# Optimization experiments

Measured on AMD Instinct MI355X. Metric: run time of the kernel, lower is better.

## Reference

```python
import math
import jax, jax.numpy as jnp
import numpy as np

B, S, D, H = 2, 4096, 512, 8
DH = D // H


def setup_inputs() -> dict:
    key = jax.random.key(0)
    ks = jax.random.split(key, 12)
    lim = 1.0 / math.sqrt(D)
    u = lambda k, shp: jax.random.uniform(k, shp, jnp.float32, -lim, lim)
    return {
        "x": jax.random.normal(ks[0], (B, S, D), jnp.float32),
        "gamma": jax.random.uniform(ks[1], (B, S, 1), jnp.float32),
        "Wq": u(ks[2], (D, D)), "bq": u(ks[3], (D,)),
        "Wk": u(ks[4], (D, D)), "bk": u(ks[5], (D,)),
        "Wv": u(ks[6], (D, D)), "bv": u(ks[7], (D,)),
        "Wo": u(ks[8], (D, D)), "bo": u(ks[9], (D,)),
    }


def reference(x, gamma, Wq, bq, Wk, bk, Wv, bv, Wo, bo):
    b, s, d = x.shape
    # projections (torch Linear: x @ W.T + b), split heads -> [B,H,S,DH]
    def proj(W, bias):
        return (x @ W.T + bias).reshape(b, s, H, DH).transpose(0, 2, 1, 3)
    q, k, v = proj(Wq, bq), proj(Wk, bk), proj(Wv, bv)

    scores = jnp.einsum("bhsd,bhtd->bhst", q, k) / math.sqrt(DH)  # [B,H,S,S]
    causal = jnp.triu(jnp.ones((s, s), bool), k=1)  # True above diagonal
    neg_inf = jnp.float32(-jnp.inf)
    scores = jnp.where(causal[None, None], neg_inf, scores)

    # hyperbolic positional bias: -log1p(gamma_i * max(i-j, 0) + 1e-8)
    pos = jnp.arange(s)
    delta = jnp.clip(pos[:, None] - pos[None, :], 0).astype(jnp.float32)  # [S,S]
    gamma_q = gamma[:, :, 0][:, :, None]  # [B,S,1]
    hyper = -jnp.log1p(gamma_q * delta + 1e-8)  # [B,S,S]
    hyper = jnp.where(causal[None], neg_inf, hyper)
    scores = scores + hyper[:, None]  # [B,H,S,S]

    attn = jax.nn.softmax(scores, axis=-1)
    out = jnp.einsum("bhst,bhtd->bhsd", attn, v)  # [B,H,S,DH]
    out = out.transpose(0, 2, 1, 3).reshape(b, s, d)
    return out @ Wo.T + bo
```

## Files before the change

kernel.cpp:

```cpp
#include <hip/hip_runtime.h>
#include <hip/hip_bf16.h>

#define Bb 2
#define Ss 4096
#define Dd 512
#define Hh 8
#define DHh 64

typedef __attribute__((ext_vector_type(8))) short short8;
typedef __attribute__((ext_vector_type(4))) float floatx4;

static __device__ __forceinline__ ushort bfbits(float f) {
  union { __hip_bfloat16 h; ushort u; } cv;
  cv.h = __float2bfloat16(f);
  return cv.u;
}

static __device__ __forceinline__ unsigned int packhi(float a, float b) {
  union { float f; unsigned int u; } ca, cb; ca.f = a; cb.f = b;
  return (ca.u >> 16) | (cb.u & 0xffff0000u);
}

__global__ void cvt_all(const float* __restrict__ x,
                        const float* __restrict__ w0, const float* __restrict__ w1,
                        const float* __restrict__ w2, const float* __restrict__ w3,
                        ushort* __restrict__ out) {
  const int XN4 = (Bb * Ss * Dd) / 4;
  const int WN4 = (Dd * Dd) / 4;
  int i = blockIdx.x * blockDim.x + threadIdx.x;
  if (i >= XN4 + 4 * WN4) return;
  const float* s; int li;
  if (i < XN4) { s = x; li = i; }
  else {
    int t = i - XN4; int j = t >> 16; li = t & (WN4 - 1);
    s = (j == 0) ? w0 : (j == 1) ? w1 : (j == 2) ? w2 : w3;
  }
  float4 f = ((const float4*)s)[li];
  ushort4 u;
  u.x = bfbits(f.x); u.y = bfbits(f.y); u.z = bfbits(f.z); u.w = bfbits(f.w);
  ((ushort4*)out)[i] = u;
}

static __device__ __forceinline__ int vperm(int s0) {
  int kb = (s0 >> 4) & 3, gq = (s0 >> 2) & 3;
  return (s0 & ~63) | ((kb >> 1) << 5) | (gq << 3) | ((kb & 1) << 2);
}

#define LDQK(buf, k0)                                                          \
  _Pragma("unroll")                                                            \
  for (int rb = 0; rb < 4; ++rb)                                               \
    af[buf][rb] = *(const short8*)(ap + (size_t)rb * 16 * 512 + (k0));         \
  _Pragma("unroll")                                                            \
  for (int cb = 0; cb < 4; ++cb)                                               \
    bf[buf][cb] = *(const short8*)(bp + (size_t)cb * 16 * 512 + (k0));

__global__ __launch_bounds__(256) void qkv_gemm(
    const ushort* __restrict__ xb,
    const ushort* __restrict__ Wq, const ushort* __restrict__ Wk, const ushort* __restrict__ Wv,
    const float* __restrict__ bq, const float* __restrict__ bk, const float* __restrict__ bv,
    ushort* __restrict__ qo, ushort* __restrict__ ko, ushort* __restrict__ vo)
{
  int mb = blockIdx.x / 12, rest = blockIdx.x % 12;
  int which = rest >> 2, nb = rest & 3;
  const ushort* Bw  = (which == 0) ? Wq : (which == 1) ? Wk : Wv;
  const float* bias = (which == 0) ? bq : (which == 1) ? bk : bv;
  int lane = threadIdx.x & 63, w = threadIdx.x >> 6;
  int wr = w & 1, wc = w >> 1;
  int g = lane >> 4, ln = lane & 15;
  int m0 = mb * 128 + wr * 64;
  int c0 = nb * 128 + wc * 64;
  const ushort* ap = xb + (size_t)(m0 + ln) * 512 + g * 8;
  const ushort* bp = Bw + (size_t)(c0 + ln) * 512 + g * 8;
  floatx4 acc[4][4] = {};
  short8 af[2][4], bf[2][4];
  LDQK(0, 0)
#pragma unroll
  for (int it = 0; it < 16; ++it) {
    int cur = it & 1;
    if (it < 15) { LDQK(cur ^ 1, (it + 1) * 32) }
#pragma unroll
    for (int rb = 0; rb < 4; ++rb)
#pragma unroll
      for (int cb = 0; cb < 4; ++cb)
        acc[rb][cb] = __builtin_amdgcn_mfma_f32_16x16x32_bf16(af[cur][rb], bf[cur][cb], acc[rb][cb], 0, 0, 0);
  }
  float scale = (which == 0) ? 0.125f : 1.0f;
#pragma unroll
  for (int rb = 0; rb < 4; ++rb)
#pragma unroll
    for (int cb = 0; cb < 4; ++cb) {
      int col = c0 + cb * 16 + ln;
      float bv_ = bias[col];
      int hh = col >> 6, dh = col & 63;
      if (which == 2) {
        int i0 = m0 + rb * 16 + g * 4;
        int bI = i0 >> 12, s0 = i0 & (Ss - 1);
        ushort4 pk;
        pk.x = bfbits(acc[rb][cb][0] + bv_);
        pk.y = bfbits(acc[rb][cb][1] + bv_);
        pk.z = bfbits(acc[rb][cb][2] + bv_);
        pk.w = bfbits(acc[rb][cb][3] + bv_);
        *(ushort4*)(vo + (((size_t)bI * Hh + hh) * DHh + dh) * Ss + vperm(s0)) = pk;
      } else {
        ushort* outp = (which == 0) ? qo : ko;
#pragma unroll
        for (int r = 0; r < 4; ++r) {
          int i = m0 + rb * 16 + g * 4 + r;
          int bI = i >> 12, s = i & (Ss - 1);
          outp[(((size_t)bI * Hh + hh) * Ss + s) * DHh + dh] = bfbits((acc[rb][cb][r] + bv_) * scale);
        }
      }
    }
}

#define LD32(buf, k0)                                                          \
  af[buf][0] = *(const short8*)(ap + (k0));                                    \
  af[buf][1] = *(const short8*)(ap + 16 * 512 + (k0));                         \
  _Pragma("unroll")                                                            \
  for (int ns = 0; ns < 4; ++ns)                                               \
    bfr[buf][ns] = *(const short8*)(bp + (size_t)ns * 16 * 512 + (k0));

__global__ __launch_bounds__(256) void gemm_out(
    const ushort* __restrict__ A, const ushort* __restrict__ Bw,
    const float* __restrict__ bias, float* __restrict__ outp)
{
  int mb = blockIdx.x >> 3, nb = blockIdx.x & 7;
  int lane = threadIdx.x & 63, w = threadIdx.x >> 6;
  int g = lane >> 4, ln = lane & 15;
  int m0 = mb * 128 + w * 32;
  const ushort* ap = A + (size_t)(m0 + ln) * 512 + g * 8;
  const ushort* bp = Bw + (size_t)(nb * 64 + ln) * 512 + g * 8;
  floatx4 acc[2][4] = {};
  short8 af[2][2], bfr[2][4];
  LD32(0, 0)
#pragma unroll
  for (int it = 0; it < 16; ++it) {
    int cur = it & 1;
    if (it < 15) { LD32(cur ^ 1, (it + 1) * 32) }
#pragma unroll
    for (int ns = 0; ns < 4; ++ns) {
      acc[0][ns] = __builtin_amdgcn_mfma_f32_16x16x32_bf16(af[cur][0], bfr[cur][ns], acc[0][ns], 0, 0, 0);
      acc[1][ns] = __builtin_amdgcn_mfma_f32_16x16x32_bf16(af[cur][1], bfr[cur][ns], acc[1][ns], 0, 0, 0);
    }
  }
#pragma unroll
  for (int rb = 0; rb < 2; ++rb)
#pragma unroll
    for (int ns = 0; ns < 4; ++ns) {
      int col = nb * 64 + ns * 16 + ln;
      float bv_ = bias[col];
#pragma unroll
      for (int r = 0; r < 4; ++r)
        outp[(size_t)(m0 + rb * 16 + g * 4 + r) * 512 + col] = acc[rb][ns][r] + bv_;
    }
}

__global__ __launch_bounds__(256, 2) void flash6(
    const ushort* __restrict__ q, const ushort* __restrict__ k,
    const ushort* __restrict__ vt, const float* __restrict__ gamma,
    ushort* __restrict__ o)
{
  __shared__ __align__(16) float Pmrg[2][64][34];
  __shared__ __align__(16) ushort Tb[2][16 * 72];

  int z = blockIdx.x;
  int bh = z & 15, up = z >> 4;
  int b = bh >> 3, hh = bh & 7;
  int tid = threadIdx.x;
  int wv = tid >> 6, lane = tid & 63;
  int qsel = wv >> 1, half = wv & 1;
  int g = lane >> 4, ln = lane & 15;

  const ushort* kp = k + ((size_t)bh * Ss + ln) * DHh + g * 8;
  const ushort* vp = vt + ((size_t)bh * DHh + ln) * Ss + g * 8;

#pragma unroll 1
  for (int rep = 0; rep < 2; ++rep) {
    int u = rep ? (63 - up) : up;
    int t = 2 * u + qsel;
    int q0 = t * 32;
    int ktm = u;
    int nkt = u + 1;
    int h = (nkt + 1 - rep) >> 1;
    int lo = half ? h : 0, hi = half ? nkt : h;

    const ushort* qp = q + ((size_t)bh * Ss + q0 + ln) * DHh + g * 8;
    short8 qf00 = *(const short8*)qp;
    short8 qf01 = *(const short8*)(qp + 32);
    short8 qf10 = *(const short8*)(qp + 16 * DHh);
    short8 qf11 = *(const short8*)(qp + 16 * DHh + 32);

    int qrow0 = q0 + ln, qrow1 = q0 + 16 + ln;
    float gm0 = gamma[(size_t)b * Ss + qrow0];
    float gm1 = gamma[(size_t)b * Ss + qrow1];
    float l2[2] = {0.0f, 0.0f};
    floatx4 oacc[2][4] = {};

    short8 kfl[4], kfh[4], vf[8];
    int kb0 = lo * 64;
#pragma unroll
    for (int ns = 0; ns < 4; ++ns) {
      kfl[ns] = *(const short8*)(kp + (size_t)(kb0 + ns * 16) * DHh);
      kfh[ns] = *(const short8*)(kp + (size_t)(kb0 + ns * 16) * DHh + 32);
    }
#pragma unroll
    for (int cc = 0; cc < 8; ++cc)
      vf[cc] = *(const short8*)(vp + (size_t)((cc & 3) * 16) * Ss + kb0 + (cc >> 2) * 32);

    for (int kt = lo; kt < hi; ++kt) {
      int kbase = kt * 64;
      float sv[2][16];
#pragma unroll
      for (int ns = 0; ns < 4; ++ns) {
        floatx4 z0 = {}, z1 = {};
        z0 = __builtin_amdgcn_mfma_f32_16x16x32_bf16(kfl[ns], qf00, z0, 0, 0, 0);
        z0 = __builtin_amdgcn_mfma_f32_16x16x32_bf16(kfh[ns], qf01, z0, 0, 0, 0);
        z1 = __builtin_amdgcn_mfma_f32_16x16x32_bf16(kfl[ns], qf10, z1, 0, 0, 0);
        z1 = __builtin_amdgcn_mfma_f32_16x16x32_bf16(kfh[ns], qf11, z1, 0, 0, 0);
#pragma unroll
        for (int r = 0; r < 4; ++r) { sv[0][ns * 4 + r] = z0[r]; sv[1][ns * 4 + r] = z1[r]; }
      }
      if (kt + 1 < hi) {
        const ushort* kn = kp + (size_t)(kbase + 64) * DHh;
#pragma unroll
        for (int ns = 0; ns < 4; ++ns) {
          kfl[ns] = *(const short8*)(kn + (size_t)(ns * 16) * DHh);
          kfh[ns] = *(const short8*)(kn + (size_t)(ns * 16) * DHh + 32);
        }
      }
      bool last = (kt == ktm);
      short8 pfrag[2][2];
#pragma unroll
      for (int qb = 0; qb < 2; ++qb) {
        int qrow = qb ? qrow1 : qrow0;
        float gm = qb ? gm1 : gm0;
        int db = qrow - kbase - g * 4;
        if (last) {
#pragma unroll
          for (int e = 0; e < 16; ++e)
            if (db - (e >> 2) * 16 - (e & 3) < 0) sv[qb][e] = -1e30f;
        }
        float fd = (float)db;
        float rs = 0.0f;
#pragma unroll
        for (int e = 0; e < 16; ++e) {
          float delta = fmaxf(fd - (float)((e >> 2) * 16 + (e & 3)), 0.0f);
          float wt = __builtin_amdgcn_rcpf(fmaf(gm, delta, 1.0f));
          float pv = __expf(sv[qb][e]) * wt;
          rs += pv;
          sv[qb][e] = pv;
        }
        l2[qb] += rs;
#pragma unroll
        for (int c = 0; c < 2; ++c) {
          uint4 pkd;
          pkd.x = packhi(sv[qb][8 * c + 0], sv[qb][8 * c + 1]);
          pkd.y = packhi(sv[qb][8 * c + 2], sv[qb][8 * c + 3]);
          pkd.z = packhi(sv[qb][8 * c + 4], sv[qb][8 * c + 5]);
          pkd.w = packhi(sv[qb][8 * c + 6], sv[qb][8 * c + 7]);
          pfrag[qb][c] = *(short8*)&pkd;
        }
      }
#pragma unroll
      for (int c = 0; c < 2; ++c)
#pragma unroll
        for (int ds = 0; ds < 4; ++ds) {
          oacc[0][ds] = __builtin_amdgcn_mfma_f32_16x16x32_bf16(vf[c * 4 + ds], pfrag[0][c], oacc[0][ds], 0, 0, 0);
          oacc[1][ds] = __builtin_amdgcn_mfma_f32_16x16x32_bf16(vf[c * 4 + ds], pfrag[1][c], oacc[1][ds], 0, 0, 0);
        }
      if (kt + 1 < hi) {
#pragma unroll
        for (int cc = 0; cc < 8; ++cc)
          vf[cc] = *(const short8*)(vp + (size_t)((cc & 3) * 16) * Ss + kbase + 64 + (cc >> 2) * 32);
      }
    }

    __syncthreads();
    if (half) {
#pragma unroll
      for (int qb = 0; qb < 2; ++qb)
#pragma unroll
        for (int ds = 0; ds < 4; ++ds)
#pragma unroll
          for (int r = 0; r < 4; ++r)
            Pmrg[qsel][lane][qb * 16 + ds * 4 + r] = oacc[qb][ds][r];
      Pmrg[qsel][lane][32] = l2[0];
      Pmrg[qsel][lane][33] = l2[1];
    }
    __syncthreads();
    if (!half) {
#pragma unroll
      for (int qb = 0; qb < 2; ++qb) {
#pragma unroll
        for (int ds = 0; ds < 4; ++ds)
#pragma unroll
          for (int r = 0; r < 4; ++r)
            oacc[qb][ds][r] += Pmrg[qsel][lane][qb * 16 + ds * 4 + r];
        float l = l2[qb] + Pmrg[qsel][lane][32 + qb];
        l += __shfl_xor(l, 16);
        l += __shfl_xor(l, 32);
        float linv = 1.0f / l;
        ushort* tb = &Tb[qsel][0];
#pragma unroll
        for (int ds = 0; ds < 4; ++ds)
#pragma unroll
          for (int r = 0; r < 4; ++r)
            tb[ln * 72 + ds * 16 + g * 4 + r] = bfbits(oacc[qb][ds][r] * linv);
        short8 v0 = *(const short8*)(tb + ln * 72 + g * 16);
        short8 v1 = *(const short8*)(tb + ln * 72 + g * 16 + 8);
        size_t oa = ((size_t)b * Ss + q0 + qb * 16 + ln) * Dd + hh * DHh + g * 16;
        *(short8*)(o + oa) = v0;
        *(short8*)(o + oa + 8) = v1;
      }
    }
  }
}

extern "C" void kernel_launch(void* const* d_in, const int* in_sizes, int n_in,
                              void* d_out, int out_size, void* d_ws, size_t ws_size,
                              hipStream_t stream) {
  const float* x     = (const float*)d_in[0];
  const float* gamma = (const float*)d_in[1];
  const float* Wq    = (const float*)d_in[2];
  const float* bq    = (const float*)d_in[3];
  const float* Wk    = (const float*)d_in[4];
  const float* bk    = (const float*)d_in[5];
  const float* Wv    = (const float*)d_in[6];
  const float* bv    = (const float*)d_in[7];
  const float* Wo    = (const float*)d_in[8];
  const float* bo    = (const float*)d_in[9];

  const size_t NX = (size_t)Bb * Ss * Dd;
  const size_t NW = (size_t)Dd * Dd;
  ushort* xb  = (ushort*)d_ws;
  ushort* Wqb = xb + NX;
  ushort* Wkb = Wqb + NW;
  ushort* Wvb = Wkb + NW;
  ushort* Wob = Wvb + NW;
  ushort* qb  = Wob + NW;
  ushort* kb  = qb + NX;
  ushort* vtb = kb + NX;
  ushort* ab  = vtb + NX;

  const int total4 = (int)(NX / 4 + 4 * (NW / 4));
  cvt_all<<<(total4 + 255) / 256, 256, 0, stream>>>(x, Wq, Wk, Wv, Wo, xb);

  qkv_gemm<<<64 * 12, 256, 0, stream>>>(xb, Wqb, Wkb, Wvb, bq, bk, bv, qb, kb, vtb);

  flash6<<<512, 256, 0, stream>>>(qb, kb, vtb, gamma, ab);

  gemm_out<<<512, 256, 0, stream>>>(ab, Wob, bo, (float*)d_out);
}
```

Measured before the change: 285.3 us.

## Split flash blocks into 128-thread tiles, use exp2 with folded scale, specialize mask path

The flash kernel moves from 256-thread blocks, each handling two query tiles over two paired reps, to 2048 blocks of 128 threads. Each block handles one 32-row query tile, and a serpentine ordering over block ids balances causal work across rounds. The Q scale now folds in log2(e) so the softmax can use a hardware exp2 instead of __expf. The non-diagonal tiles skip masking and the delta clamp, and the row sum is split into four partial accumulators to shorten the dependency chain. Smaller blocks give finer scheduling granularity and less barrier coupling, but they rely on block dispatch order for load balance.

```diff
diff --git a/kernel.cpp b/kernel.cpp
--- a/kernel.cpp
+++ b/kernel.cpp
@@ -84,7 +84,7 @@
       for (int cb = 0; cb < 4; ++cb)
         acc[rb][cb] = __builtin_amdgcn_mfma_f32_16x16x32_bf16(af[cur][rb], bf[cur][cb], acc[rb][cb], 0, 0, 0);
   }
-  float scale = (which == 0) ? 0.125f : 1.0f;
+  float scale = (which == 0) ? 0.18033688011112042f : 1.0f;
 #pragma unroll
   for (int rb = 0; rb < 4; ++rb)
 #pragma unroll
@@ -155,163 +155,169 @@
     }
 }
 
-__global__ __launch_bounds__(256, 2) void flash6(
+__global__ __launch_bounds__(128, 4) void flash7(
     const ushort* __restrict__ q, const ushort* __restrict__ k,
     const ushort* __restrict__ vt, const float* __restrict__ gamma,
     ushort* __restrict__ o)
 {
-  __shared__ __align__(16) float Pmrg[2][64][34];
-  __shared__ __align__(16) ushort Tb[2][16 * 72];
+  __shared__ __align__(16) float Pmrg[64][34];
+  __shared__ __align__(16) ushort Tb[16 * 72];
 
   int z = blockIdx.x;
-  int bh = z & 15, up = z >> 4;
+  int bh = z & 15;
   int b = bh >> 3, hh = bh & 7;
+  int sslot = (z >> 4) & 15, rnd = z >> 8;
+  int j = (rnd << 4) | ((rnd & 1) ? (15 - sslot) : sslot);
+  int u = j >> 1, qsel = j & 1;
+
   int tid = threadIdx.x;
-  int wv = tid >> 6, lane = tid & 63;
-  int qsel = wv >> 1, half = wv & 1;
+  int half = tid >> 6, lane = tid & 63;
   int g = lane >> 4, ln = lane & 15;
 
   const ushort* kp = k + ((size_t)bh * Ss + ln) * DHh + g * 8;
   const ushort* vp = vt + ((size_t)bh * DHh + ln) * Ss + g * 8;
 
-#pragma unroll 1
-  for (int rep = 0; rep < 2; ++rep) {
-    int u = rep ? (63 - up) : up;
-    int t = 2 * u + qsel;
-    int q0 = t * 32;
-    int ktm = u;
-    int nkt = u + 1;
-    int h = (nkt + 1 - rep) >> 1;
-    int lo = half ? h : 0, hi = half ? nkt : h;
-
-    const ushort* qp = q + ((size_t)bh * Ss + q0 + ln) * DHh + g * 8;
-    short8 qf00 = *(const short8*)qp;
-    short8 qf01 = *(const short8*)(qp + 32);
-    short8 qf10 = *(const short8*)(qp + 16 * DHh);
-    short8 qf11 = *(const short8*)(qp + 16 * DHh + 32);
-
-    int qrow0 = q0 + ln, qrow1 = q0 + 16 + ln;
-    float gm0 = gamma[(size_t)b * Ss + qrow0];
-    float gm1 = gamma[(size_t)b * Ss + qrow1];
-    float l2[2] = {0.0f, 0.0f};
-    floatx4 oacc[2][4] = {};
-
-    short8 kfl[4], kfh[4], vf[8];
-    int kb0 = lo * 64;
+  int t = 2 * u + qsel;
+  int q0 = t * 32;
+  int ktm = u;
+  int nkt = u + 1;
+  int h = nkt >> 1;
+  int lo = half ? h : 0, hi = half ? nkt : h;
+
+  const ushort* qp = q + ((size_t)bh * Ss + q0 + ln) * DHh + g * 8;
+  short8 qf00 = *(const short8*)qp;
+  short8 qf01 = *(const short8*)(qp + 32);
+  short8 qf10 = *(const short8*)(qp + 16 * DHh);
+  short8 qf11 = *(const short8*)(qp + 16 * DHh + 32);
+
+  int qrow0 = q0 + ln, qrow1 = q0 + 16 + ln;
+  float gm0 = gamma[(size_t)b * Ss + qrow0];
+  float gm1 = gamma[(size_t)b * Ss + qrow1];
+  float l2[2] = {0.0f, 0.0f};
+  floatx4 oacc[2][4] = {};
+
+  short8 kfl[4], kfh[4], vf[8];
+  int kb0 = lo * 64;
+#pragma unroll
+  for (int ns = 0; ns < 4; ++ns) {
+    kfl[ns] = *(const short8*)(kp + (size_t)(kb0 + ns * 16) * DHh);
+    kfh[ns] = *(const short8*)(kp + (size_t)(kb0 + ns * 16) * DHh + 32);
+  }
+#pragma unroll
+  for (int cc = 0; cc < 8; ++cc)
+    vf[cc] = *(const short8*)(vp + (size_t)((cc & 3) * 16) * Ss + kb0 + (cc >> 2) * 32);
+
+  for (int kt = lo; kt < hi; ++kt) {
+    int kbase = kt * 64;
+    float sv[2][16];
 #pragma unroll
     for (int ns = 0; ns < 4; ++ns) {
-      kfl[ns] = *(const short8*)(kp + (size_t)(kb0 + ns * 16) * DHh);
-      kfh[ns] = *(const short8*)(kp + (size_t)(kb0 + ns * 16) * DHh + 32);
-    }
-#pragma unroll
-    for (int cc = 0; cc < 8; ++cc)
-      vf[cc] = *(const short8*)(vp + (size_t)((cc & 3) * 16) * Ss + kb0 + (cc >> 2) * 32);
-
-    for (int kt = lo; kt < hi; ++kt) {
-      int kbase = kt * 64;
-      float sv[2][16];
+      floatx4 z0 = {}, z1 = {};
+      z0 = __builtin_amdgcn_mfma_f32_16x16x32_bf16(kfl[ns], qf00, z0, 0, 0, 0);
+      z0 = __builtin_amdgcn_mfma_f32_16x16x32_bf16(kfh[ns], qf01, z0, 0, 0, 0);
+      z1 = __builtin_amdgcn_mfma_f32_16x16x32_bf16(kfl[ns], qf10, z1, 0, 0, 0);
+      z1 = __builtin_amdgcn_mfma_f32_16x16x32_bf16(kfh[ns], qf11, z1, 0, 0, 0);
+#pragma unroll
+      for (int r = 0; r < 4; ++r) { sv[0][ns * 4 + r] = z0[r]; sv[1][ns * 4 + r] = z1[r]; }
+    }
+    if (kt + 1 < hi) {
+      const ushort* kn = kp + (size_t)(kbase + 64) * DHh;
 #pragma unroll
       for (int ns = 0; ns < 4; ++ns) {
-        floatx4 z0 = {}, z1 = {};
-        z0 = __builtin_amdgcn_mfma_f32_16x16x32_bf16(kfl[ns], qf00, z0, 0, 0, 0);
-        z0 = __builtin_amdgcn_mfma_f32_16x16x32_bf16(kfh[ns], qf01, z0, 0, 0, 0);
-        z1 = __builtin_amdgcn_mfma_f32_16x16x32_bf16(kfl[ns], qf10, z1, 0, 0, 0);
-        z1 = __builtin_amdgcn_mfma_f32_16x16x32_bf16(kfh[ns], qf11, z1, 0, 0, 0);
-#pragma unroll
-        for (int r = 0; r < 4; ++r) { sv[0][ns * 4 + r] = z0[r]; sv[1][ns * 4 + r] = z1[r]; }
-      }
-      if (kt + 1 < hi) {
-        const ushort* kn = kp + (size_t)(kbase + 64) * DHh;
-#pragma unroll
-        for (int ns = 0; ns < 4; ++ns) {
-          kfl[ns] = *(const short8*)(kn + (size_t)(ns * 16) * DHh);
-          kfh[ns] = *(const short8*)(kn + (size_t)(ns * 16) * DHh + 32);
-        }
-      }
-      bool last = (kt == ktm);
-      short8 pfrag[2][2];
-#pragma unroll
-      for (int qb = 0; qb < 2; ++qb) {
-        int qrow = qb ? qrow1 : qrow0;
-        float gm = qb ? gm1 : gm0;
-        int db = qrow - kbase - g * 4;
-        if (last) {
-#pragma unroll
-          for (int e = 0; e < 16; ++e)
-            if (db - (e >> 2) * 16 - (e & 3) < 0) sv[qb][e] = -1e30f;
-        }
-        float fd = (float)db;
-        float rs = 0.0f;
+        kfl[ns] = *(const short8*)(kn + (size_t)(ns * 16) * DHh);
+        kfh[ns] = *(const short8*)(kn + (size_t)(ns * 16) * DHh + 32);
+      }
+    }
+    bool last = (kt == ktm);
+    short8 pfrag[2][2];
+#pragma unroll
+    for (int qb = 0; qb < 2; ++qb) {
+      int qrow = qb ? qrow1 : qrow0;
+      float gm = qb ? gm1 : gm0;
+      int db = qrow - kbase - g * 4;
+      float fd = (float)db;
+      float rsub[4] = {0.0f, 0.0f, 0.0f, 0.0f};
+      if (last) {
 #pragma unroll
         for (int e = 0; e < 16; ++e) {
-          float delta = fmaxf(fd - (float)((e >> 2) * 16 + (e & 3)), 0.0f);
+          int off = (e >> 2) * 16 + (e & 3);
+          if (db - off < 0) sv[qb][e] = -1e30f;
+          float delta = fmaxf(fd - (float)off, 0.0f);
           float wt = __builtin_amdgcn_rcpf(fmaf(gm, delta, 1.0f));
-          float pv = __expf(sv[qb][e]) * wt;
-          rs += pv;
+          float pv = __builtin_amdgcn_exp2f(sv[qb][e]) * wt;
+          rsub[e & 3] += pv;
           sv[qb][e] = pv;
         }
-        l2[qb] += rs;
-#pragma unroll
-        for (int c = 0; c < 2; ++c) {
-          uint4 pkd;
-          pkd.x = packhi(sv[qb][8 * c + 0], sv[qb][8 * c + 1]);
-          pkd.y = packhi(sv[qb][8 * c + 2], sv[qb][8 * c + 3]);
-          pkd.z = packhi(sv[qb][8 * c + 4], sv[qb][8 * c + 5]);
-          pkd.w = packhi(sv[qb][8 * c + 6], sv[qb][8 * c + 7]);
-          pfrag[qb][c] = *(short8*)&pkd;
+      } else {
+#pragma unroll
+        for (int e = 0; e < 16; ++e) {
+          float delta = fd - (float)((e >> 2) * 16 + (e & 3));
+          float wt = __builtin_amdgcn_rcpf(fmaf(gm, delta, 1.0f));
+          float pv = __builtin_amdgcn_exp2f(sv[qb][e]) * wt;
+          rsub[e & 3] += pv;
+          sv[qb][e] = pv;
         }
       }
-#pragma unroll
-      for (int c = 0; c < 2; ++c)
-#pragma unroll
-        for (int ds = 0; ds < 4; ++ds) {
-          oacc[0][ds] = __builtin_amdgcn_mfma_f32_16x16x32_bf16(vf[c * 4 + ds], pfrag[0][c], oacc[0][ds], 0, 0, 0);
-          oacc[1][ds] = __builtin_amdgcn_mfma_f32_16x16x32_bf16(vf[c * 4 + ds], pfrag[1][c], oacc[1][ds], 0, 0, 0);
-        }
-      if (kt + 1 < hi) {
-#pragma unroll
-        for (int cc = 0; cc < 8; ++cc)
-          vf[cc] = *(const short8*)(vp + (size_t)((cc & 3) * 16) * Ss + kbase + 64 + (cc >> 2) * 32);
-      }
-    }
-
-    __syncthreads();
-    if (half) {
-#pragma unroll
-      for (int qb = 0; qb < 2; ++qb)
-#pragma unroll
-        for (int ds = 0; ds < 4; ++ds)
-#pragma unroll
-          for (int r = 0; r < 4; ++r)
-            Pmrg[qsel][lane][qb * 16 + ds * 4 + r] = oacc[qb][ds][r];
-      Pmrg[qsel][lane][32] = l2[0];
-      Pmrg[qsel][lane][33] = l2[1];
-    }
-    __syncthreads();
-    if (!half) {
-#pragma unroll
-      for (int qb = 0; qb < 2; ++qb) {
-#pragma unroll
-        for (int ds = 0; ds < 4; ++ds)
-#pragma unroll
-          for (int r = 0; r < 4; ++r)
-            oacc[qb][ds][r] += Pmrg[qsel][lane][qb * 16 + ds * 4 + r];
-        float l = l2[qb] + Pmrg[qsel][lane][32 + qb];
-        l += __shfl_xor(l, 16);
-        l += __shfl_xor(l, 32);
-        float linv = 1.0f / l;
-        ushort* tb = &Tb[qsel][0];
-#pragma unroll
-        for (int ds = 0; ds < 4; ++ds)
-#pragma unroll
-          for (int r = 0; r < 4; ++r)
-            tb[ln * 72 + ds * 16 + g * 4 + r] = bfbits(oacc[qb][ds][r] * linv);
-        short8 v0 = *(const short8*)(tb + ln * 72 + g * 16);
-        short8 v1 = *(const short8*)(tb + ln * 72 + g * 16 + 8);
-        size_t oa = ((size_t)b * Ss + q0 + qb * 16 + ln) * Dd + hh * DHh + g * 16;
-        *(short8*)(o + oa) = v0;
-        *(short8*)(o + oa + 8) = v1;
-      }
+      l2[qb] += (rsub[0] + rsub[1]) + (rsub[2] + rsub[3]);
+#pragma unroll
+      for (int c = 0; c < 2; ++c) {
+        uint4 pkd;
+        pkd.x = packhi(sv[qb][8 * c + 0], sv[qb][8 * c + 1]);
+        pkd.y = packhi(sv[qb][8 * c + 2], sv[qb][8 * c + 3]);
+        pkd.z = packhi(sv[qb][8 * c + 4], sv[qb][8 * c + 5]);
+        pkd.w = packhi(sv[qb][8 * c + 6], sv[qb][8 * c + 7]);
+        pfrag[qb][c] = *(short8*)&pkd;
+      }
+    }
+#pragma unroll
+    for (int c = 0; c < 2; ++c)
+#pragma unroll
+      for (int ds = 0; ds < 4; ++ds) {
+        oacc[0][ds] = __builtin_amdgcn_mfma_f32_16x16x32_bf16(vf[c * 4 + ds], pfrag[0][c], oacc[0][ds], 0, 0, 0);
+        oacc[1][ds] = __builtin_amdgcn_mfma_f32_16x16x32_bf16(vf[c * 4 + ds], pfrag[1][c], oacc[1][ds], 0, 0, 0);
+      }
+    if (kt + 1 < hi) {
+#pragma unroll
+      for (int cc = 0; cc < 8; ++cc)
+        vf[cc] = *(const short8*)(vp + (size_t)((cc & 3) * 16) * Ss + kbase + 64 + (cc >> 2) * 32);
+    }
+  }
+
+  if (half) {
+#pragma unroll
+    for (int qb = 0; qb < 2; ++qb)
+#pragma unroll
+      for (int ds = 0; ds < 4; ++ds)
+#pragma unroll
+        for (int r = 0; r < 4; ++r)
+          Pmrg[lane][qb * 16 + ds * 4 + r] = oacc[qb][ds][r];
+    Pmrg[lane][32] = l2[0];
+    Pmrg[lane][33] = l2[1];
+  }
+  __syncthreads();
+  if (!half) {
+#pragma unroll
+    for (int qb = 0; qb < 2; ++qb) {
+#pragma unroll
+      for (int ds = 0; ds < 4; ++ds)
+#pragma unroll
+        for (int r = 0; r < 4; ++r)
+          oacc[qb][ds][r] += Pmrg[lane][qb * 16 + ds * 4 + r];
+      float l = l2[qb] + Pmrg[lane][32 + qb];
+      l += __shfl_xor(l, 16);
+      l += __shfl_xor(l, 32);
+      float linv = 1.0f / l;
+      ushort* tb = &Tb[0];
+#pragma unroll
+      for (int ds = 0; ds < 4; ++ds)
+#pragma unroll
+        for (int r = 0; r < 4; ++r)
+          tb[ln * 72 + ds * 16 + g * 4 + r] = bfbits(oacc[qb][ds][r] * linv);
+      short8 v0 = *(const short8*)(tb + ln * 72 + g * 16);
+      short8 v1 = *(const short8*)(tb + ln * 72 + g * 16 + 8);
+      size_t oa = ((size_t)b * Ss + q0 + qb * 16 + ln) * Dd + hh * DHh + g * 16;
+      *(short8*)(o + oa) = v0;
+      *(short8*)(o + oa + 8) = v1;
     }
   }
 }
@@ -347,7 +353,7 @@
 
   qkv_gemm<<<64 * 12, 256, 0, stream>>>(xb, Wqb, Wkb, Wvb, bq, bk, bv, qb, kb, vtb);
 
-  flash6<<<512, 256, 0, stream>>>(qb, kb, vtb, gamma, ab);
+  flash7<<<2048, 128, 0, stream>>>(qb, kb, vtb, gamma, ab);
 
   gemm_out<<<512, 256, 0, stream>>>(ab, Wob, bo, (float*)d_out);
 }
```

Result: slower. 551.8 us (+93.4%).

## Split attention key range across three waves per query tile with exp2 softmax

Applied to the files above, without the earlier changes.

The attention kernel now gives each block a single 32-row query tile, with three waves splitting that tile's key range and merging their partial results through shared memory. Previously two query tiles were each split two ways, and the grid doubles to 1024 blocks of 192 threads. The Q scale now folds in log2(e) so the softmax can use exp2 directly, and non-diagonal tiles skip the causal mask and the clamp. V fragments are loaded on demand rather than prefetched, which lowers register pressure at the cost of exposed load latency.

```diff
diff --git a/kernel.cpp b/kernel.cpp
--- a/kernel.cpp
+++ b/kernel.cpp
@@ -84,7 +84,7 @@
       for (int cb = 0; cb < 4; ++cb)
         acc[rb][cb] = __builtin_amdgcn_mfma_f32_16x16x32_bf16(af[cur][rb], bf[cur][cb], acc[rb][cb], 0, 0, 0);
   }
-  float scale = (which == 0) ? 0.125f : 1.0f;
+  float scale = (which == 0) ? 0.18033688011112042f : 1.0f;
 #pragma unroll
   for (int rb = 0; rb < 4; ++rb)
 #pragma unroll
@@ -155,20 +155,22 @@
     }
 }
 
-__global__ __launch_bounds__(256, 2) void flash6(
+__global__ __launch_bounds__(192) void flash12(
     const ushort* __restrict__ q, const ushort* __restrict__ k,
     const ushort* __restrict__ vt, const float* __restrict__ gamma,
     ushort* __restrict__ o)
 {
   __shared__ __align__(16) float Pmrg[2][64][34];
-  __shared__ __align__(16) ushort Tb[2][16 * 72];
+  __shared__ __align__(16) ushort Tb[16 * 72];
 
   int z = blockIdx.x;
-  int bh = z & 15, up = z >> 4;
+  int bh = z & 15;
   int b = bh >> 3, hh = bh & 7;
+  int qsel = (z >> 4) & 1;
+  int up = z >> 5;
+
   int tid = threadIdx.x;
   int wv = tid >> 6, lane = tid & 63;
-  int qsel = wv >> 1, half = wv & 1;
   int g = lane >> 4, ln = lane & 15;
 
   const ushort* kp = k + ((size_t)bh * Ss + ln) * DHh + g * 8;
@@ -177,12 +179,12 @@
 #pragma unroll 1
   for (int rep = 0; rep < 2; ++rep) {
     int u = rep ? (63 - up) : up;
-    int t = 2 * u + qsel;
-    int q0 = t * 32;
+    int nkt = u + 1;
     int ktm = u;
-    int nkt = u + 1;
-    int h = (nkt + 1 - rep) >> 1;
-    int lo = half ? h : 0, hi = half ? nkt : h;
+    int qd = nkt / 3, rr = nkt % 3;
+    int lo = wv * qd + (wv < rr ? wv : rr);
+    int hi = lo + qd + (wv < rr ? 1 : 0);
+    int q0 = (2 * u + qsel) * 32;
 
     const ushort* qp = q + ((size_t)bh * Ss + q0 + ln) * DHh + g * 8;
     short8 qf00 = *(const short8*)qp;
@@ -196,111 +198,118 @@
     float l2[2] = {0.0f, 0.0f};
     floatx4 oacc[2][4] = {};
 
-    short8 kfl[4], kfh[4], vf[8];
-    int kb0 = lo * 64;
-#pragma unroll
-    for (int ns = 0; ns < 4; ++ns) {
-      kfl[ns] = *(const short8*)(kp + (size_t)(kb0 + ns * 16) * DHh);
-      kfh[ns] = *(const short8*)(kp + (size_t)(kb0 + ns * 16) * DHh + 32);
-    }
-#pragma unroll
-    for (int cc = 0; cc < 8; ++cc)
-      vf[cc] = *(const short8*)(vp + (size_t)((cc & 3) * 16) * Ss + kb0 + (cc >> 2) * 32);
-
-    for (int kt = lo; kt < hi; ++kt) {
-      int kbase = kt * 64;
-      float sv[2][16];
+    if (lo < hi) {
+      short8 kfl[4], kfh[4];
+      int kb0 = lo * 64;
 #pragma unroll
       for (int ns = 0; ns < 4; ++ns) {
-        floatx4 z0 = {}, z1 = {};
-        z0 = __builtin_amdgcn_mfma_f32_16x16x32_bf16(kfl[ns], qf00, z0, 0, 0, 0);
-        z0 = __builtin_amdgcn_mfma_f32_16x16x32_bf16(kfh[ns], qf01, z0, 0, 0, 0);
-        z1 = __builtin_amdgcn_mfma_f32_16x16x32_bf16(kfl[ns], qf10, z1, 0, 0, 0);
-        z1 = __builtin_amdgcn_mfma_f32_16x16x32_bf16(kfh[ns], qf11, z1, 0, 0, 0);
-#pragma unroll
-        for (int r = 0; r < 4; ++r) { sv[0][ns * 4 + r] = z0[r]; sv[1][ns * 4 + r] = z1[r]; }
+        kfl[ns] = *(const short8*)(kp + (size_t)(kb0 + ns * 16) * DHh);
+        kfh[ns] = *(const short8*)(kp + (size_t)(kb0 + ns * 16) * DHh + 32);
       }
-      if (kt + 1 < hi) {
-        const ushort* kn = kp + (size_t)(kbase + 64) * DHh;
-#pragma unroll
-        for (int ns = 0; ns < 4; ++ns) {
-          kfl[ns] = *(const short8*)(kn + (size_t)(ns * 16) * DHh);
-          kfh[ns] = *(const short8*)(kn + (size_t)(ns * 16) * DHh + 32);
+
+      for (int kt = lo; kt < hi; ++kt) {
+        int kbase = kt * 64;
+        bool last = (kt == ktm);
+        short8 pfrag[2][2];
+#pragma unroll
+        for (int qb = 0; qb < 2; ++qb) {
+          short8 qlo = qb ? qf10 : qf00;
+          short8 qhi = qb ? qf11 : qf01;
+          int qrow = qb ? qrow1 : qrow0;
+          float gm = qb ? gm1 : gm0;
+          int db = qrow - kbase - g * 4;
+          float fd = (float)db;
+          float base = fmaf(gm, fd, 1.0f);
+#pragma unroll
+          for (int nsg = 0; nsg < 2; ++nsg) {
+            floatx4 za = {}, zb = {};
+            za = __builtin_amdgcn_mfma_f32_16x16x32_bf16(kfl[2 * nsg + 0], qlo, za, 0, 0, 0);
+            za = __builtin_amdgcn_mfma_f32_16x16x32_bf16(kfh[2 * nsg + 0], qhi, za, 0, 0, 0);
+            zb = __builtin_amdgcn_mfma_f32_16x16x32_bf16(kfl[2 * nsg + 1], qlo, zb, 0, 0, 0);
+            zb = __builtin_amdgcn_mfma_f32_16x16x32_bf16(kfh[2 * nsg + 1], qhi, zb, 0, 0, 0);
+            float f[8];
+#pragma unroll
+            for (int r = 0; r < 4; ++r) { f[r] = za[r]; f[4 + r] = zb[r]; }
+            float rs0 = 0.0f, rs1 = 0.0f;
+            if (last) {
+#pragma unroll
+              for (int e = 0; e < 8; ++e) {
+                int off = nsg * 32 + (e >> 2) * 16 + (e & 3);
+                if (db - off < 0) f[e] = -1e30f;
+                float delta = fmaxf(fd - (float)off, 0.0f);
+                float wt = __builtin_amdgcn_rcpf(fmaf(gm, delta, 1.0f));
+                float pv = __builtin_amdgcn_exp2f(f[e]) * wt;
+                if (e & 1) rs1 += pv; else rs0 += pv;
+                f[e] = pv;
+              }
+            } else {
+#pragma unroll
+              for (int e = 0; e < 8; ++e) {
+                float off = (float)(nsg * 32 + (e >> 2) * 16 + (e & 3));
+                float wt = __builtin_amdgcn_rcpf(fmaf(gm, -off, base));
+                float pv = __builtin_amdgcn_exp2f(f[e]) * wt;
+                if (e & 1) rs1 += pv; else rs0 += pv;
+                f[e] = pv;
+              }
+            }
+            l2[qb] += rs0 + rs1;
+            uint4 pkd;
+            pkd.x = packhi(f[0], f[1]);
+            pkd.y = packhi(f[2], f[3]);
+            pkd.z = packhi(f[4], f[5]);
+            pkd.w = packhi(f[6], f[7]);
+            pfrag[qb][nsg] = *(short8*)&pkd;
+          }
+        }
+        if (kt + 1 < hi) {
+          const ushort* kn = kp + (size_t)(kbase + 64) * DHh;
+#pragma unroll
+          for (int ns = 0; ns < 4; ++ns) {
+            kfl[ns] = *(const short8*)(kn + (size_t)(ns * 16) * DHh);
+            kfh[ns] = *(const short8*)(kn + (size_t)(ns * 16) * DHh + 32);
+          }
+        }
+#pragma unroll
+        for (int c = 0; c < 2; ++c) {
+          short8 vfg[4];
+#pragma unroll
+          for (int ds = 0; ds < 4; ++ds)
+            vfg[ds] = *(const short8*)(vp + (size_t)(ds * 16) * Ss + kbase + c * 32);
+#pragma unroll
+          for (int ds = 0; ds < 4; ++ds) {
+            oacc[0][ds] = __builtin_amdgcn_mfma_f32_16x16x32_bf16(vfg[ds], pfrag[0][c], oacc[0][ds], 0, 0, 0);
+            oacc[1][ds] = __builtin_amdgcn_mfma_f32_16x16x32_bf16(vfg[ds], pfrag[1][c], oacc[1][ds], 0, 0, 0);
+          }
         }
       }
-      bool last = (kt == ktm);
-      short8 pfrag[2][2];
+    }
+
+    if (wv) {
+#pragma unroll
+      for (int qb = 0; qb < 2; ++qb)
+#pragma unroll
+        for (int ds = 0; ds < 4; ++ds)
+#pragma unroll
+          for (int r = 0; r < 4; ++r)
+            Pmrg[wv - 1][lane][qb * 16 + ds * 4 + r] = oacc[qb][ds][r];
+      Pmrg[wv - 1][lane][32] = l2[0];
+      Pmrg[wv - 1][lane][33] = l2[1];
+    }
+    __syncthreads();
+    if (wv == 0) {
 #pragma unroll
       for (int qb = 0; qb < 2; ++qb) {
-        int qrow = qb ? qrow1 : qrow0;
-        float gm = qb ? gm1 : gm0;
-        int db = qrow - kbase - g * 4;
-        if (last) {
-#pragma unroll
-          for (int e = 0; e < 16; ++e)
-            if (db - (e >> 2) * 16 - (e & 3) < 0) sv[qb][e] = -1e30f;
-        }
-        float fd = (float)db;
-        float rs = 0.0f;
-#pragma unroll
-        for (int e = 0; e < 16; ++e) {
-          float delta = fmaxf(fd - (float)((e >> 2) * 16 + (e & 3)), 0.0f);
-          float wt = __builtin_amdgcn_rcpf(fmaf(gm, delta, 1.0f));
-          float pv = __expf(sv[qb][e]) * wt;
-          rs += pv;
-          sv[qb][e] = pv;
-        }
-        l2[qb] += rs;
-#pragma unroll
-        for (int c = 0; c < 2; ++c) {
-          uint4 pkd;
-          pkd.x = packhi(sv[qb][8 * c + 0], sv[qb][8 * c + 1]);
-          pkd.y = packhi(sv[qb][8 * c + 2], sv[qb][8 * c + 3]);
-          pkd.z = packhi(sv[qb][8 * c + 4], sv[qb][8 * c + 5]);
-          pkd.w = packhi(sv[qb][8 * c + 6], sv[qb][8 * c + 7]);
-          pfrag[qb][c] = *(short8*)&pkd;
-        }
-      }
-#pragma unroll
-      for (int c = 0; c < 2; ++c)
-#pragma unroll
-        for (int ds = 0; ds < 4; ++ds) {
-          oacc[0][ds] = __builtin_amdgcn_mfma_f32_16x16x32_bf16(vf[c * 4 + ds], pfrag[0][c], oacc[0][ds], 0, 0, 0);
-          oacc[1][ds] = __builtin_amdgcn_mfma_f32_16x16x32_bf16(vf[c * 4 + ds], pfrag[1][c], oacc[1][ds], 0, 0, 0);
-        }
-      if (kt + 1 < hi) {
-#pragma unroll
-        for (int cc = 0; cc < 8; ++cc)
-          vf[cc] = *(const short8*)(vp + (size_t)((cc & 3) * 16) * Ss + kbase + 64 + (cc >> 2) * 32);
-      }
-    }
-
-    __syncthreads();
-    if (half) {
-#pragma unroll
-      for (int qb = 0; qb < 2; ++qb)
 #pragma unroll
         for (int ds = 0; ds < 4; ++ds)
 #pragma unroll
           for (int r = 0; r < 4; ++r)
-            Pmrg[qsel][lane][qb * 16 + ds * 4 + r] = oacc[qb][ds][r];
-      Pmrg[qsel][lane][32] = l2[0];
-      Pmrg[qsel][lane][33] = l2[1];
-    }
-    __syncthreads();
-    if (!half) {
-#pragma unroll
-      for (int qb = 0; qb < 2; ++qb) {
-#pragma unroll
-        for (int ds = 0; ds < 4; ++ds)
-#pragma unroll
-          for (int r = 0; r < 4; ++r)
-            oacc[qb][ds][r] += Pmrg[qsel][lane][qb * 16 + ds * 4 + r];
-        float l = l2[qb] + Pmrg[qsel][lane][32 + qb];
+            oacc[qb][ds][r] += Pmrg[0][lane][qb * 16 + ds * 4 + r]
+                             + Pmrg[1][lane][qb * 16 + ds * 4 + r];
+        float l = l2[qb] + Pmrg[0][lane][32 + qb] + Pmrg[1][lane][32 + qb];
         l += __shfl_xor(l, 16);
         l += __shfl_xor(l, 32);
         float linv = 1.0f / l;
-        ushort* tb = &Tb[qsel][0];
+        ushort* tb = &Tb[0];
 #pragma unroll
         for (int ds = 0; ds < 4; ++ds)
 #pragma unroll
@@ -313,6 +322,7 @@
         *(short8*)(o + oa + 8) = v1;
       }
     }
+    __syncthreads();
   }
 }
 
@@ -347,7 +357,7 @@
 
   qkv_gemm<<<64 * 12, 256, 0, stream>>>(xb, Wqb, Wkb, Wvb, bq, bk, bv, qb, kb, vtb);
 
-  flash6<<<512, 256, 0, stream>>>(qb, kb, vtb, gamma, ab);
+  flash12<<<1024, 192, 0, stream>>>(qb, kb, vtb, gamma, ab);
 
   gemm_out<<<512, 256, 0, stream>>>(ab, Wob, bo, (float*)d_out);
 }
```

Result: no change. 286.9 us (+0.6%).
